# Optimization experiments

Hardware: AMD Instinct MI355X
Metric: run time of the kernel (lower is better)

The kernel has to match this reference:

```python
import jax, jax.numpy as jnp
import numpy as np

BS, T, FIN, FOUT = 8, 1024, 512, 512
ALPHA = 0.1      # leaky relu slope
T_K = 3          # t_ksize (odd); temporal band radius = T_K // 2
S_K = 4          # s_ksize semantic topk
NEG_INF = -9e15


def setup_inputs() -> dict:
    key = jax.random.key(0)
    k1, k2, k3, k4 = jax.random.split(key, 4)
    # xavier-uniform-ish scales (gain 1.414)
    w_lim = 1.414 * np.sqrt(6.0 / (FIN + FOUT))
    a_lim = 1.414 * np.sqrt(6.0 / (2 * FOUT + 1))
    return {
        "x_a": jax.random.normal(k1, (BS, T, FIN), jnp.float32),
        "x_v": jax.random.normal(k2, (BS, T, FIN), jnp.float32),
        "W": jax.random.uniform(k3, (FIN, FOUT), jnp.float32, -w_lim, w_lim),
        "a": jax.random.uniform(k4, (2 * FOUT, 1), jnp.float32, -a_lim, a_lim),
    }


def _temporal_mask(t):
    # tem_adj[i,j] = 1 iff |i-j| <= T_K//2 and i, j on the same side of t-0.5
    idx = jnp.arange(2 * t)
    same_side = (idx[:, None] >= t) == (idx[None, :] >= t)
    band = jnp.abs(idx[:, None] - idx[None, :]) <= (T_K // 2)
    return band & same_side  # (2t, 2t) bool


def _semantic_block_mask(x, k):
    # x: (bs, t, d). Top-k neighbors by negative squared euclidean distance.
    inner = 2.0 * jnp.einsum("btd,bsd->bts", x, x)
    sq = jnp.sum(x * x, axis=-1, keepdims=True)  # (bs, t, 1)
    pd = -(sq - inner + jnp.swapaxes(sq, -1, -2))  # (bs, t, t)
    _, idx = jax.lax.top_k(pd, k)  # (bs, t, k)
    bs, t = x.shape[0], x.shape[1]
    b_ix = jnp.arange(bs)[:, None, None]
    r_ix = jnp.arange(t)[None, :, None]
    return jnp.zeros((bs, t, t), bool).at[b_ix, r_ix, idx].set(True)


def reference(x_a, x_v, W, a):
    bs, t, _ = x_a.shape
    h = jnp.concatenate([x_a, x_v], axis=1)          # (bs, 2t, FIN)
    Wh = h @ W                                        # (bs, 2t, FOUT)

    # additive GAT score: e = leakyrelu(Wh a1 + (Wh a2)^T)
    Wh1 = Wh @ a[:FOUT]                               # (bs, 2t, 1)
    Wh2 = Wh @ a[FOUT:]                               # (bs, 2t, 1)
    e = Wh1 + jnp.swapaxes(Wh2, -1, -2)               # (bs, 2t, 2t)
    e = jnp.where(e > 0, e, ALPHA * e)                # leaky relu

    # adjacency: temporal band + semantic topk within aa / vv blocks
    tem = _temporal_mask(t)                           # (2t, 2t)
    sem_aa = _semantic_block_mask(Wh[:, :t], S_K)     # (bs, t, t)
    sem_vv = _semantic_block_mask(Wh[:, t:], S_K)     # (bs, t, t)
    zb = jnp.zeros((bs, t, t), bool)
    sem = jnp.concatenate([
        jnp.concatenate([sem_aa, zb], axis=-1),
        jnp.concatenate([zb, sem_vv], axis=-1),
    ], axis=1)                                        # (bs, 2t, 2t)
    mask = tem[None] | sem

    attention = jax.nn.softmax(jnp.where(mask, e, NEG_INF), axis=-1)
    h_prime = jax.nn.elu(attention @ Wh)              # (bs, 2t, FOUT)
    return h_prime[:, :t], h_prime[:, t:]
```

## Files before the change

### kernel.cpp

```cpp
#include <hip/hip_runtime.h>
#include <math.h>

#define T_ 1024
#define BS_ 8
#define D_ 512
#define NROWS_ (BS_*2*T_)
#define ALPHA_ 0.1f

typedef _Float16 f16;
typedef _Float16 f16x8 __attribute__((ext_vector_type(8)));
typedef _Float16 f16x4 __attribute__((ext_vector_type(4)));
typedef _Float16 f16x2 __attribute__((ext_vector_type(2)));
typedef float f32x4 __attribute__((ext_vector_type(4)));

#define MFMA16(A,B,C) __builtin_amdgcn_mfma_f32_16x16x32_f16((A),(B),(C),0,0,0)

__device__ __forceinline__ void gl16(const void* g, void* l) {
    __builtin_amdgcn_global_load_lds(
        (const __attribute__((address_space(1))) unsigned int*)g,
        (__attribute__((address_space(3))) unsigned int*)l, 16, 0, 0);
}

#if __has_builtin(__builtin_amdgcn_fdot2)
__device__ __forceinline__ float fdot2p(f16x2 a, f16x2 b, float c) {
    return __builtin_amdgcn_fdot2(a, b, c, false);
}
#else
__device__ __forceinline__ float fdot2p(f16x2 a, f16x2 b, float c) {
    return fmaf((float)a[1], (float)b[1], fmaf((float)a[0], (float)b[0], c));
}
#endif

__device__ __forceinline__ float fdot8(const f16x8 a, const f16x8 b, float s) {
    #pragma unroll
    for (int q = 0; q < 4; ++q) {
        f16x2 aa, bb;
        aa[0] = a[2*q]; aa[1] = a[2*q+1];
        bb[0] = b[2*q]; bb[1] = b[2*q+1];
        s = fdot2p(aa, bb, s);
    }
    return s;
}

__device__ __forceinline__ unsigned sortable(float f) {
    unsigned u = __float_as_uint(f);
    return u ^ ((u & 0x80000000u) ? 0xFFFFFFFFu : 0x80000000u);
}
__device__ __forceinline__ unsigned pack_key(float s, int col) {
    return (sortable(s) & 0xFFFFFC00u) | (unsigned)(1023 - col);
}

#define INSK4(K, X) { \
    bool g3 = (X) > K[3], g2 = (X) > K[2], g1 = (X) > K[1], g0 = (X) > K[0]; \
    K[3] = g2 ? K[2] : (g3 ? (X) : K[3]); \
    K[2] = g1 ? K[1] : (g2 ? (X) : K[2]); \
    K[1] = g0 ? K[0] : (g1 ? (X) : K[1]); \
    K[0] = g0 ? (X) : K[0]; }

#define INSK8(K, X) { \
    bool h7=(X)>K[7],h6=(X)>K[6],h5=(X)>K[5],h4=(X)>K[4]; \
    bool h3=(X)>K[3],h2=(X)>K[2],h1=(X)>K[1],h0=(X)>K[0]; \
    K[7]=h6?K[6]:(h7?(X):K[7]); K[6]=h5?K[5]:(h6?(X):K[6]); \
    K[5]=h4?K[4]:(h5?(X):K[5]); K[4]=h3?K[3]:(h4?(X):K[4]); \
    K[3]=h2?K[2]:(h3?(X):K[3]); K[2]=h1?K[1]:(h2?(X):K[2]); \
    K[1]=h0?K[0]:(h1?(X):K[1]); K[0]=h0?(X):K[0]; }

#define CEU(a,b) { unsigned mx_ = (a) > (b) ? (a) : (b); \
    unsigned mn_ = (a) > (b) ? (b) : (a); (a) = mx_; (b) = mn_; }

#define MERGE8(K, MSK) { \
    unsigned b0=__shfl_xor(K[0],MSK), b1=__shfl_xor(K[1],MSK), \
             b2=__shfl_xor(K[2],MSK), b3=__shfl_xor(K[3],MSK), \
             b4=__shfl_xor(K[4],MSK), b5=__shfl_xor(K[5],MSK), \
             b6=__shfl_xor(K[6],MSK), b7=__shfl_xor(K[7],MSK); \
    K[0]=K[0]>b7?K[0]:b7; K[1]=K[1]>b6?K[1]:b6; \
    K[2]=K[2]>b5?K[2]:b5; K[3]=K[3]>b4?K[3]:b4; \
    K[4]=K[4]>b3?K[4]:b3; K[5]=K[5]>b2?K[5]:b2; \
    K[6]=K[6]>b1?K[6]:b1; K[7]=K[7]>b0?K[7]:b0; \
    CEU(K[0],K[4]); CEU(K[1],K[5]); CEU(K[2],K[6]); CEU(K[3],K[7]); \
    CEU(K[0],K[2]); CEU(K[1],K[3]); CEU(K[4],K[6]); CEU(K[5],K[7]); \
    CEU(K[0],K[1]); CEU(K[2],K[3]); CEU(K[4],K[5]); CEU(K[6],K[7]); }

#define BETTER(x,xi,v,vi) ((x) > (v) || ((x) == (v) && (xi) < (vi)))
#define INS4T(TV,TI,X,ID) { \
    bool g3 = BETTER(X,ID,TV[3],TI[3]), g2 = BETTER(X,ID,TV[2],TI[2]); \
    bool g1 = BETTER(X,ID,TV[1],TI[1]), g0 = BETTER(X,ID,TV[0],TI[0]); \
    TV[3] = g2 ? TV[2] : (g3 ? (X) : TV[3]); TI[3] = g2 ? TI[2] : (g3 ? (ID) : TI[3]); \
    TV[2] = g1 ? TV[1] : (g2 ? (X) : TV[2]); TI[2] = g1 ? TI[1] : (g2 ? (ID) : TI[2]); \
    TV[1] = g0 ? TV[0] : (g1 ? (X) : TV[1]); TI[1] = g0 ? TI[0] : (g1 ? (ID) : TI[1]); \
    TV[0] = g0 ? (X) : TV[0]; TI[0] = g0 ? (ID) : TI[0]; }

__global__ __launch_bounds__(256) void k_splitW(
    const float* __restrict__ W, f16* __restrict__ WTh, f16* __restrict__ WTl)
{
    __shared__ float tile[64][65];
    const int tid = threadIdx.x;
    const int tk = (blockIdx.x >> 3) << 6, tn = (blockIdx.x & 7) << 6;
    const int r0 = tid >> 4, c4 = (tid & 15) << 2;

    #pragma unroll
    for (int rr = 0; rr < 4; ++rr) {
        int k = r0 + (rr << 4);
        float4 v = *(const float4*)(W + (size_t)(tk + k) * D_ + tn + c4);
        tile[k][c4+0] = v.x; tile[k][c4+1] = v.y;
        tile[k][c4+2] = v.z; tile[k][c4+3] = v.w;
    }
    __syncthreads();
    #pragma unroll
    for (int rr = 0; rr < 4; ++rr) {
        int n = r0 + (rr << 4);
        f16x4 h, l;
        #pragma unroll
        for (int i = 0; i < 4; ++i) {
            float x = tile[c4 + i][n];
            f16 hh = (f16)x; h[i] = hh; l[i] = (f16)(x - (float)hh);
        }
        *(f16x4*)(WTh + (size_t)(tn + n) * D_ + tk + c4) = h;
        *(f16x4*)(WTl + (size_t)(tn + n) * D_ + tk + c4) = l;
    }
}

__global__ __launch_bounds__(512, 4) void k_gemm_wh(
    const float* __restrict__ xa, const float* __restrict__ xv,
    const f16* __restrict__ WTh, const f16* __restrict__ WTl,
    const float* __restrict__ a,
    f16* __restrict__ Whh, f16* __restrict__ Whl,
    float* __restrict__ stP)
{
    __shared__ __align__(16) unsigned char smem[69632];

    const int tid  = threadIdx.x;
    const int w    = tid >> 6;
    const int wr   = w >> 2, wc = w & 3;
    const int lane = tid & 63;
    const int l15  = lane & 15;
    const int g    = lane >> 4;
    const int bid  = blockIdx.x;
    const int swz  = ((bid & 7) << 6) + (bid >> 3);
    const int rowbase = (swz >> 1) << 6;
    const int nt   = swz & 1;

    if (tid < 256)
        *(float4*)(smem + 65536 + (tid << 4)) = *(const float4*)(a + (tid << 2));

    const int qp = rowbase >> 10;
    const float* xsrc = ((qp & 1) ? xv : xa)
                      + (size_t)((qp >> 1) * 1024 + (rowbase & 1023)) * D_;
    const int arow = (wr << 5) + l15;

    const char* WThB = (const char*)WTh;
    const char* WTlB = (const char*)WTl;

    const int col0 = tid >> 3;
    const int j80  = (tid & 7) ^ (col0 & 7);

    const int bo0 = (((wc << 5) +  0 + l15) << 7) + ((g ^ (l15 & 7)) << 4);
    const int bo1 = (((wc << 5) + 16 + l15) << 7) + ((g ^ (l15 & 7)) << 4);

    #define STAGE_B(t_) { \
        const int kc_ = (t_) >> 1, cq_ = (t_) & 1; \
        const int bufb_ = ((t_) & 1) << 15; \
        const size_t g0_ = ((size_t)((nt << 8) + (cq_ << 7) + col0) << 10) + ((size_t)kc_ << 7) + (j80 << 4); \
        const size_t g1_ = g0_ + ((size_t)64 << 10); \
        gl16(WThB + g0_, smem + bufb_ + (tid << 4)); \
        gl16(WThB + g1_, smem + bufb_ + ((tid + 512) << 4)); \
        gl16(WTlB + g0_, smem + bufb_ + 16384 + (tid << 4)); \
        gl16(WTlB + g1_, smem + bufb_ + 16384 + ((tid + 512) << 4)); }

    #define LOAD_A(dst_, kc_) { \
        _Pragma("unroll") \
        for (int r_ = 0; r_ < 2; ++r_) { \
            const float* p_ = xsrc + (size_t)(arow + (r_ << 4)) * D_ + ((kc_) << 6) + (g << 3); \
            dst_[(r_ << 2) + 0] = *(const float4*)(p_); \
            dst_[(r_ << 2) + 1] = *(const float4*)(p_ + 4); \
            dst_[(r_ << 2) + 2] = *(const float4*)(p_ + 32); \
            dst_[(r_ << 2) + 3] = *(const float4*)(p_ + 36); } }

    #define CONV_A(src_) { \
        _Pragma("unroll") \
        for (int r_ = 0; r_ < 2; ++r_) \
        _Pragma("unroll") \
        for (int s_ = 0; s_ < 2; ++s_) { \
            float4 v0_ = src_[(r_ << 2) + (s_ << 1)]; \
            float4 v1_ = src_[(r_ << 2) + (s_ << 1) + 1]; \
            float xs_[8] = {v0_.x,v0_.y,v0_.z,v0_.w,v1_.x,v1_.y,v1_.z,v1_.w}; \
            f16x8 h_, l_; \
            _Pragma("unroll") \
            for (int e_ = 0; e_ < 8; ++e_) { \
                f16 hh_ = (f16)xs_[e_]; h_[e_] = hh_; l_[e_] = (f16)(xs_[e_] - (float)hh_); } \
            AH[r_][s_] = h_; AL[r_][s_] = l_; } }

    f32x4 acc[2][2][2];
    #pragma unroll
    for (int cq = 0; cq < 2; ++cq)
        #pragma unroll
        for (int m = 0; m < 2; ++m)
            #pragma unroll
            for (int c = 0; c < 2; ++c) acc[cq][m][c] = (f32x4){0.f,0.f,0.f,0.f};

    float4 aR[8];
    f16x8 AH[2][2], AL[2][2];

    LOAD_A(aR, 0);
    STAGE_B(0);

    #pragma unroll
    for (int t = 0; t < 16; ++t) {
        const int kc = t >> 1, cq = t & 1, bufb = (t & 1) << 15;
        __syncthreads();
        if (t < 15) STAGE_B(t + 1);
        if (cq == 0) { CONV_A(aR); }
        else if (kc < 7) { LOAD_A(aR, kc + 1); }

        #pragma unroll
        for (int s = 0; s < 2; ++s) {
            const int sx = s << 6;
            f16x8 bh0 = *(const f16x8*)(smem + bufb + (bo0 ^ sx));
            f16x8 bh1 = *(const f16x8*)(smem + bufb + (bo1 ^ sx));
            f16x8 bl0 = *(const f16x8*)(smem + bufb + 16384 + (bo0 ^ sx));
            f16x8 bl1 = *(const f16x8*)(smem + bufb + 16384 + (bo1 ^ sx));

            acc[cq][0][0] = MFMA16(AH[0][s], bh0, acc[cq][0][0]);
            acc[cq][0][1] = MFMA16(AH[0][s], bh1, acc[cq][0][1]);
            acc[cq][1][0] = MFMA16(AH[1][s], bh0, acc[cq][1][0]);
            acc[cq][1][1] = MFMA16(AH[1][s], bh1, acc[cq][1][1]);
            acc[cq][0][0] = MFMA16(AL[0][s], bh0, acc[cq][0][0]);
            acc[cq][0][1] = MFMA16(AL[0][s], bh1, acc[cq][0][1]);
            acc[cq][1][0] = MFMA16(AL[1][s], bh0, acc[cq][1][0]);
            acc[cq][1][1] = MFMA16(AL[1][s], bh1, acc[cq][1][1]);
            acc[cq][0][0] = MFMA16(AH[0][s], bl0, acc[cq][0][0]);
            acc[cq][0][1] = MFMA16(AH[0][s], bl1, acc[cq][0][1]);
            acc[cq][1][0] = MFMA16(AH[1][s], bl0, acc[cq][1][0]);
            acc[cq][1][1] = MFMA16(AH[1][s], bl1, acc[cq][1][1]);
        }
    }
    #undef STAGE_B
    #undef LOAD_A
    #undef CONV_A

    __syncthreads();

    float st1[8], st2[8], stq[8];
    #pragma unroll
    for (int s = 0; s < 8; ++s) { st1[s] = 0.f; st2[s] = 0.f; stq[s] = 0.f; }

    #pragma unroll
    for (int cq = 0; cq < 2; ++cq)
        #pragma unroll
        for (int c = 0; c < 2; ++c) {
            const int col = (nt << 8) + (cq << 7) + (wc << 5) + (c << 4) + l15;
            const float a1 = *(const float*)(smem + 65536 + (col << 2));
            const float a2 = *(const float*)(smem + 65536 + 2048 + (col << 2));
            #pragma unroll
            for (int m = 0; m < 2; ++m)
                #pragma unroll
                for (int j = 0; j < 4; ++j) {
                    const float v = acc[cq][m][c][j];
                    const int slot = (m << 2) + j;
                    st1[slot] = fmaf(v, a1, st1[slot]);
                    st2[slot] = fmaf(v, a2, st2[slot]);
                    stq[slot] = fmaf(v, v,  stq[slot]);
                    f16 h = (f16)v; f16 l = (f16)(v - (float)h);
                    const size_t off = (size_t)(rowbase + (wr << 5) + (m << 4) + (g << 2) + j) * D_ + col;
                    Whh[off] = h; Whl[off] = l;
                }
        }

    #pragma unroll
    for (int mask = 1; mask < 16; mask <<= 1)
        #pragma unroll
        for (int s = 0; s < 8; ++s) {
            st1[s] += __shfl_xor(st1[s], mask);
            st2[s] += __shfl_xor(st2[s], mask);
            stq[s] += __shfl_xor(stq[s], mask);
        }
    if (l15 == 0) {
        #pragma unroll
        for (int s = 0; s < 8; ++s) {
            const int rl = (wr << 5) + ((s >> 2) << 4) + (g << 2) + (s & 3);
            float* sp = (float*)smem + ((rl << 2) + wc) * 3;
            sp[0] = st1[s]; sp[1] = st2[s]; sp[2] = stq[s];
        }
    }
    __syncthreads();
    if (tid < 64) {
        float s1 = 0.f, s2 = 0.f, s3 = 0.f;
        #pragma unroll
        for (int wv = 0; wv < 4; ++wv) {
            const float* sp = (const float*)smem + ((tid << 2) + wv) * 3;
            s1 += sp[0]; s2 += sp[1]; s3 += sp[2];
        }
        float* base = stP + (size_t)nt * 3 * NROWS_;
        base[rowbase + tid]              = s1;
        base[NROWS_ + rowbase + tid]     = s2;
        base[2 * NROWS_ + rowbase + tid] = s3;
    }
}

__global__ __launch_bounds__(256) void k_stats(
    const float* __restrict__ stP, float* __restrict__ Wh1,
    float* __restrict__ Wh2, float* __restrict__ sq)
{
    const int i = (blockIdx.x << 8) + threadIdx.x;
    const float* p0 = stP;
    const float* p1 = stP + 3 * NROWS_;
    Wh1[i] = p0[i] + p1[i];
    Wh2[i] = p0[NROWS_ + i] + p1[NROWS_ + i];
    sq[i]  = p0[2 * NROWS_ + i] + p1[2 * NROWS_ + i];
}

__global__ __launch_bounds__(512, 1) void k_gram_topk8(
    const f16* __restrict__ Whh, const float* __restrict__ sq,
    int* __restrict__ topk8)
{
    __shared__ __align__(16) unsigned char smem[81920];

    const int bid = blockIdx.x;
    const int swz = ((bid & 7) << 5) + (bid >> 3);
    const int p   = swz >> 4;
    const int rt  = swz & 15;
    const int rowbase  = (p << 10) + (rt << 6);
    const int colPanel = p << 10;

    const int tid  = threadIdx.x;
    const int w    = tid >> 6;
    const int wr   = w >> 2, wc = w & 3;
    const int lane = tid & 63;
    const int l15  = lane & 15;
    const int g    = lane >> 4;
    const int r8   = lane >> 3;
    const int k7   = lane & 7;
    const int sw2  = ((k7 ^ r8) << 4);
    const int q0x  = ((g ^ (lane & 7)) << 4);

    const int rowA = tid >> 3;
    const int k7A  = tid & 7;
    const int aswz = ((k7A ^ (rowA & 7)) << 4);

    const char* WB = (const char*)Whh;

    const int aoff0 = 32768 + (((wr << 5) +  0 + l15) << 7) + q0x;
    const int aoff1 = 32768 + (((wr << 5) + 16 + l15) << 7) + q0x;
    const int boff0 = (((wc << 6) +  0 + l15) << 7) + q0x;
    const int boff1 = (((wc << 6) + 16 + l15) << 7) + q0x;
    const int boff2 = (((wc << 6) + 32 + l15) << 7) + q0x;
    const int boff3 = (((wc << 6) + 48 + l15) << 7) + q0x;

    f32x4 acc[2][4];
    #pragma unroll
    for (int m = 0; m < 2; ++m)
        #pragma unroll
        for (int c = 0; c < 4; ++c) acc[m][c] = (f32x4){0.f,0.f,0.f,0.f};

    unsigned k4[8][4];
    #pragma unroll
    for (int s = 0; s < 8; ++s)
        #pragma unroll
        for (int q = 0; q < 4; ++q) k4[s][q] = 0u;

    #define STAGE_G(t) { \
        const int ct_ = (t) >> 3, kc_ = (t) & 7; \
        const int bufb_ = ((t) & 1) * 40960; \
        size_t gB_ = ((size_t)(colPanel + (ct_ << 8) + (w << 5) + r8) << 10) + (kc_ << 7) + sw2; \
        int ldsB_ = bufb_ + (w << 12) + (lane << 4); \
        _Pragma("unroll") \
        for (int j_ = 0; j_ < 4; ++j_) { \
            gl16(WB + gB_, smem + ldsB_); \
            gB_ += (size_t)8 << 10; ldsB_ += 1024; \
        } \
        size_t gA_ = ((size_t)(rowbase + rowA) << 10) + (kc_ << 7) + aswz; \
        gl16(WB + gA_, smem + bufb_ + 32768 + (tid << 4)); \
    }

    STAGE_G(0);

    for (int t = 0; t < 32; ++t) {
        __syncthreads();
        if (t < 31) STAGE_G(t + 1);
        const int bufb = (t & 1) * 40960;

        #pragma unroll
        for (int s = 0; s < 2; ++s) {
            const int sx = s << 6;
            f16x8 a0 = *(const f16x8*)(smem + bufb + (aoff0 ^ sx));
            f16x8 a1 = *(const f16x8*)(smem + bufb + (aoff1 ^ sx));
            f16x8 b0 = *(const f16x8*)(smem + bufb + (boff0 ^ sx));
            f16x8 b1 = *(const f16x8*)(smem + bufb + (boff1 ^ sx));
            f16x8 b2 = *(const f16x8*)(smem + bufb + (boff2 ^ sx));
            f16x8 b3 = *(const f16x8*)(smem + bufb + (boff3 ^ sx));
            acc[0][0] = MFMA16(a0, b0, acc[0][0]);
            acc[0][1] = MFMA16(a0, b1, acc[0][1]);
            acc[0][2] = MFMA16(a0, b2, acc[0][2]);
            acc[0][3] = MFMA16(a0, b3, acc[0][3]);
            acc[1][0] = MFMA16(a1, b0, acc[1][0]);
            acc[1][1] = MFMA16(a1, b1, acc[1][1]);
            acc[1][2] = MFMA16(a1, b2, acc[1][2]);
            acc[1][3] = MFMA16(a1, b3, acc[1][3]);
        }

        if ((t & 7) == 7) {
            const int ct = t >> 3;
            #pragma unroll
            for (int c = 0; c < 4; ++c) {
                const int cl = (ct << 8) + (wc << 6) + (c << 4) + l15;
                const float sqc = sq[colPanel + cl];
                #pragma unroll
                for (int m = 0; m < 2; ++m)
                    #pragma unroll
                    for (int j = 0; j < 4; ++j) {
                        float sc = fmaf(2.f, acc[m][c][j], -sqc);
                        unsigned key = pack_key(sc, cl);
                        INSK4(k4[(m << 2) + j], key);
                    }
                acc[0][c] = (f32x4){0.f,0.f,0.f,0.f};
                acc[1][c] = (f32x4){0.f,0.f,0.f,0.f};
            }
        }
    }

    unsigned k8[8][8];
    #pragma unroll
    for (int s = 0; s < 8; ++s) {
        #pragma unroll
        for (int q = 0; q < 4; ++q) { k8[s][q] = k4[s][q]; k8[s][4 + q] = 0u; }
    }
    #pragma unroll
    for (int msk = 1; msk < 16; msk <<= 1) {
        #pragma unroll
        for (int s = 0; s < 8; ++s) { MERGE8(k8[s], msk); }
    }

    if (l15 == 0) {
        #pragma unroll
        for (int s = 0; s < 8; ++s) {
            const int row_local = ((s >> 2) << 4) + (g << 2) + (s & 3);
            const int off = ((((wr << 5) + row_local) << 2) + wc) << 5;
            *(uint4*)(smem + off)      = make_uint4(k8[s][0], k8[s][1], k8[s][2], k8[s][3]);
            *(uint4*)(smem + off + 16) = make_uint4(k8[s][4], k8[s][5], k8[s][6], k8[s][7]);
        }
    }
    __syncthreads();
    if (tid < 64) {
        const unsigned* bp = (const unsigned*)smem + (tid << 5);
        unsigned kk[8];
        #pragma unroll
        for (int s = 0; s < 8; ++s) kk[s] = bp[s];
        #pragma unroll
        for (int wv = 1; wv < 4; ++wv)
            #pragma unroll
            for (int s = 0; s < 8; ++s) { unsigned x = bp[(wv << 3) + s]; INSK8(kk, x); }
        #pragma unroll
        for (int s = 0; s < 8; ++s)
            topk8[(((size_t)(rowbase + tid)) << 3) + s] = 1023 - (int)(kk[s] & 1023u);
    }
    #undef STAGE_G
}

__global__ __launch_bounds__(256) void k_rescore_agg(
    const f16* __restrict__ Whh, const f16* __restrict__ Whl,
    const float* __restrict__ Wh1, const float* __restrict__ Wh2,
    const float* __restrict__ sq, const int* __restrict__ topk8,
    float* __restrict__ out)
{
    const int bid = blockIdx.x;
    const int swz = ((bid & 7) << 9) + (bid >> 3);
    const int tid  = threadIdx.x;
    const int lane = tid & 63;
    const int r    = (swz << 2) + (tid >> 6);
    const int p    = r >> 10;
    const int i    = r & 1023;
    const int rb   = p << 10;

    const size_t ro = (size_t)r * D_ + (lane << 3);
    f16x8 ah = *(const f16x8*)(Whh + ro);
    f16x8 al = *(const f16x8*)(Whl + ro);

    int cid[8];
    {
        int4 t0 = *(const int4*)(topk8 + ((size_t)r << 3));
        int4 t1 = *(const int4*)(topk8 + ((size_t)r << 3) + 4);
        cid[0]=t0.x; cid[1]=t0.y; cid[2]=t0.z; cid[3]=t0.w;
        cid[4]=t1.x; cid[5]=t1.y; cid[6]=t1.z; cid[7]=t1.w;
    }

    float dp[8];
    #pragma unroll
    for (int c = 0; c < 8; ++c) {
        const size_t co = (size_t)(rb + cid[c]) * D_ + (lane << 3);
        f16x8 bh = *(const f16x8*)(Whh + co);
        f16x8 bl = *(const f16x8*)(Whl + co);
        float s = 0.f;
        s = fdot8(ah, bh, s);
        s = fdot8(ah, bl, s);
        s = fdot8(al, bh, s);
        dp[c] = s;
    }
    #pragma unroll
    for (int off = 32; off > 0; off >>= 1)
        #pragma unroll
        for (int c = 0; c < 8; ++c) dp[c] += __shfl_xor(dp[c], off);

    float tv[4] = {-3.4e38f,-3.4e38f,-3.4e38f,-3.4e38f};
    int   ti[4] = {0x7FFFFFFF,0x7FFFFFFF,0x7FFFFFFF,0x7FFFFFFF};
    #pragma unroll
    for (int c = 0; c < 8; ++c) {
        float sc = fmaf(2.f, dp[c], -sq[rb + cid[c]]);
        INS4T(tv, ti, sc, cid[c]);
    }

    const int  tM = i - 1, tC = i, tP = i + 1;
    const bool vM = (i > 0), vP = (i < T_ - 1);
    const int s0 = ti[0], s1 = ti[1], s2 = ti[2], s3 = ti[3];

    bool u0 = !((vM && s0 == tM) || (s0 == tC) || (vP && s0 == tP));
    bool u1 = !((vM && s1 == tM) || (s1 == tC) || (vP && s1 == tP));
    bool u2 = !((vM && s2 == tM) || (s2 == tC) || (vP && s2 == tP));
    bool u3 = !((vM && s3 == tM) || (s3 == tC) || (vP && s3 == tP));

    int  ci[7] = { vM ? tM : 0, tC, vP ? tP : 0, s0, s1, s2, s3 };
    bool cv[7] = { vM, true, vP, u0, u1, u2, u3 };

    const float e1 = Wh1[r];
    float ev[7];
    float m = -3.4e38f;
    #pragma unroll
    for (int q = 0; q < 7; ++q) {
        float e = e1 + Wh2[rb + ci[q]];
        e = (e > 0.f) ? e : ALPHA_ * e;
        e = cv[q] ? e : -3.4e38f;
        ev[q] = e;
        m = fmaxf(m, e);
    }
    float wsum = 0.f;
    #pragma unroll
    for (int q = 0; q < 7; ++q) {
        float wq = cv[q] ? expf(ev[q] - m) : 0.f;
        ev[q] = wq;
        wsum += wq;
    }
    #pragma unroll
    for (int q = 0; q < 7; ++q) ev[q] /= wsum;

    float A[8] = {0.f,0.f,0.f,0.f,0.f,0.f,0.f,0.f};
    #pragma unroll
    for (int q = 0; q < 7; ++q) {
        if (ev[q] > 0.f) {
            const float wq = ev[q];
            const size_t qo = (size_t)(rb + ci[q]) * D_ + (lane << 3);
            f16x8 vh = *(const f16x8*)(Whh + qo);
            f16x8 vl = *(const f16x8*)(Whl + qo);
            #pragma unroll
            for (int e = 0; e < 8; ++e) A[e] = fmaf(wq, (float)vh[e], A[e]);
            #pragma unroll
            for (int e = 0; e < 8; ++e) A[e] = fmaf(wq, (float)vl[e], A[e]);
        }
    }
    #pragma unroll
    for (int e = 0; e < 8; ++e)
        A[e] = (A[e] > 0.f) ? A[e] : expm1f(A[e]);

    const int blk = p & 1, b = p >> 1;
    float* dst = out + (size_t)blk * ((size_t)BS_ * T_ * D_)
               + ((size_t)((b << 10) + i)) * D_ + (lane << 3);
    *(float4*)(dst)     = make_float4(A[0], A[1], A[2], A[3]);
    *(float4*)(dst + 4) = make_float4(A[4], A[5], A[6], A[7]);
}

extern "C" void kernel_launch(void* const* d_in, const int* in_sizes, int n_in,
                              void* d_out, int out_size, void* d_ws, size_t ws_size,
                              hipStream_t stream)
{
    const float* xa = (const float*)d_in[0];
    const float* xv = (const float*)d_in[1];
    const float* W  = (const float*)d_in[2];
    const float* a  = (const float*)d_in[3];
    float* out = (float*)d_out;

    f16* Whh    = (f16*)d_ws;
    f16* Whl    = Whh + (size_t)NROWS_ * D_;
    f16* WTh    = Whl + (size_t)NROWS_ * D_;
    f16* WTl    = WTh + (size_t)D_ * D_;
    float* Wh1  = (float*)(WTl + (size_t)D_ * D_);
    float* Wh2  = Wh1 + NROWS_;
    float* sq   = Wh2 + NROWS_;
    int* topk8  = (int*)(sq + NROWS_);
    float* stP  = (float*)(topk8 + ((size_t)NROWS_ << 3));

    k_splitW     <<<dim3(64),   dim3(256), 0, stream>>>(W, WTh, WTl);
    k_gemm_wh    <<<dim3(512),  dim3(512), 0, stream>>>(xa, xv, WTh, WTl, a, Whh, Whl, stP);
    k_stats      <<<dim3(64),   dim3(256), 0, stream>>>(stP, Wh1, Wh2, sq);
    k_gram_topk8 <<<dim3(256),  dim3(512), 0, stream>>>(Whh, sq, topk8);
    k_rescore_agg<<<dim3(4096), dim3(256), 0, stream>>>(Whh, Whl, Wh1, Wh2, sq, topk8, out);
}
```

Measured before the change: 131.6 us.

## Widen GEMM tile to full 512 columns and drop separate stats kernel

Each GEMM block now computes a 64-row by full 512-column tile instead of half the columns, so per-row statistics (Wh·a1, Wh·a2, squared norm) are reduced entirely inside the block and the separate k_stats kernel and partial-stat buffer go away. The A operand is now converted to hi/lo fp16 once and staged through LDS, shared across both column halves, rather than held in registers per wave. The aim is to halve redundant A loads and conversions and remove one launch. In exchange the grid halves to 256 blocks, LDS use and registers per block grow, and occupancy bounds drop to 2 blocks per CU.

```diff
diff --git a/kernel.cpp b/kernel.cpp
--- a/kernel.cpp
+++ b/kernel.cpp
@@ -120,14 +120,14 @@
     }
 }
 
-__global__ __launch_bounds__(512, 4) void k_gemm_wh(
+__global__ __launch_bounds__(512, 2) void k_gemm_wh(
     const float* __restrict__ xa, const float* __restrict__ xv,
     const f16* __restrict__ WTh, const f16* __restrict__ WTl,
     const float* __restrict__ a,
     f16* __restrict__ Whh, f16* __restrict__ Whl,
-    float* __restrict__ stP)
+    float* __restrict__ Wh1, float* __restrict__ Wh2, float* __restrict__ sq)
 {
-    __shared__ __align__(16) unsigned char smem[69632];
+    __shared__ __align__(16) unsigned char smem[86016];
 
     const int tid  = threadIdx.x;
     const int w    = tid >> 6;
@@ -136,135 +136,146 @@
     const int l15  = lane & 15;
     const int g    = lane >> 4;
     const int bid  = blockIdx.x;
-    const int swz  = ((bid & 7) << 6) + (bid >> 3);
-    const int rowbase = (swz >> 1) << 6;
-    const int nt   = swz & 1;
+    const int swz  = ((bid & 7) << 5) + (bid >> 3);
+    const int rowbase = swz << 6;
 
     if (tid < 256)
-        *(float4*)(smem + 65536 + (tid << 4)) = *(const float4*)(a + (tid << 2));
+        *(float4*)(smem + 81920 + (tid << 4)) = *(const float4*)(a + (tid << 2));
 
     const int qp = rowbase >> 10;
     const float* xsrc = ((qp & 1) ? xv : xa)
                       + (size_t)((qp >> 1) * 1024 + (rowbase & 1023)) * D_;
-    const int arow = (wr << 5) + l15;
 
     const char* WThB = (const char*)WTh;
     const char* WTlB = (const char*)WTl;
 
-    const int col0 = tid >> 3;
-    const int j80  = (tid & 7) ^ (col0 & 7);
-
-    const int bo0 = (((wc << 5) +  0 + l15) << 7) + ((g ^ (l15 & 7)) << 4);
-    const int bo1 = (((wc << 5) + 16 + l15) << 7) + ((g ^ (l15 & 7)) << 4);
-
-    #define STAGE_B(t_) { \
-        const int kc_ = (t_) >> 1, cq_ = (t_) & 1; \
-        const int bufb_ = ((t_) & 1) << 15; \
-        const size_t g0_ = ((size_t)((nt << 8) + (cq_ << 7) + col0) << 10) + ((size_t)kc_ << 7) + (j80 << 4); \
-        const size_t g1_ = g0_ + ((size_t)64 << 10); \
-        gl16(WThB + g0_, smem + bufb_ + (tid << 4)); \
-        gl16(WThB + g1_, smem + bufb_ + ((tid + 512) << 4)); \
-        gl16(WTlB + g0_, smem + bufb_ + 16384 + (tid << 4)); \
-        gl16(WTlB + g1_, smem + bufb_ + 16384 + ((tid + 512) << 4)); }
-
-    #define LOAD_A(dst_, kc_) { \
+    const int rB1 = tid >> 2,         cB1 = tid & 3;
+    const int jB1 = cB1 ^ ((rB1 >> 1) & 3);
+    const int rB2 = (tid + 512) >> 2, cB2 = tid & 3;
+    const int jB2 = cB2 ^ ((rB2 >> 1) & 3);
+
+    const int rowA = tid >> 3, c8 = tid & 7;
+    const int aW = (rowA << 6) + ((((c8 >> 1) ^ ((rowA >> 1) & 3)) << 4)) + ((c8 & 1) << 3);
+
+    const int swzx = (g ^ ((l15 >> 1) & 3)) << 4;
+    const int ao0 = (((wr << 5) + l15) << 6) + swzx;
+    const int ao1 = ao0 + 1024;
+    const int bo0 = (((wc << 6) +  0 + l15) << 6) + swzx;
+    const int bo1 = (((wc << 6) + 16 + l15) << 6) + swzx;
+    const int bo2 = (((wc << 6) + 32 + l15) << 6) + swzx;
+    const int bo3 = (((wc << 6) + 48 + l15) << 6) + swzx;
+
+    #define STAGE_B(cq_, kc_, bufb_) { \
+        size_t g1_ = ((size_t)(((cq_) << 8) + rB1) << 10) + ((size_t)(kc_) << 6) + (jB1 << 4); \
+        size_t g2_ = ((size_t)(((cq_) << 8) + rB2) << 10) + ((size_t)(kc_) << 6) + (jB2 << 4); \
+        gl16(WThB + g1_, smem + (bufb_) + (tid << 4)); \
+        gl16(WThB + g2_, smem + (bufb_) + ((tid + 512) << 4)); \
+        gl16(WTlB + g1_, smem + (bufb_) + 16384 + (tid << 4)); \
+        gl16(WTlB + g2_, smem + (bufb_) + 16384 + ((tid + 512) << 4)); }
+
+    #define STAGE_A(kc_) { \
+        float4 v_ = *(const float4*)(xsrc + (size_t)rowA * D_ + ((kc_) << 5) + (c8 << 2)); \
+        float xs_[4] = {v_.x, v_.y, v_.z, v_.w}; \
+        f16x4 h_, l_; \
         _Pragma("unroll") \
-        for (int r_ = 0; r_ < 2; ++r_) { \
-            const float* p_ = xsrc + (size_t)(arow + (r_ << 4)) * D_ + ((kc_) << 6) + (g << 3); \
-            dst_[(r_ << 2) + 0] = *(const float4*)(p_); \
-            dst_[(r_ << 2) + 1] = *(const float4*)(p_ + 4); \
-            dst_[(r_ << 2) + 2] = *(const float4*)(p_ + 32); \
-            dst_[(r_ << 2) + 3] = *(const float4*)(p_ + 36); } }
-
-    #define CONV_A(src_) { \
+        for (int e_ = 0; e_ < 4; ++e_) { \
+            f16 hh_ = (f16)xs_[e_]; h_[e_] = hh_; l_[e_] = (f16)(xs_[e_] - (float)hh_); } \
+        const int ab_ = 65536 + (((kc_) & 1) << 13); \
+        *(f16x4*)(smem + ab_ + aW)        = h_; \
+        *(f16x4*)(smem + ab_ + 4096 + aW) = l_; }
+
+    #define COMPUTE(ACC, BUFB, AB) { \
+        f16x8 ah0 = *(const f16x8*)(smem + (AB) + ao0); \
+        f16x8 ah1 = *(const f16x8*)(smem + (AB) + ao1); \
+        f16x8 al0 = *(const f16x8*)(smem + (AB) + 4096 + ao0); \
+        f16x8 al1 = *(const f16x8*)(smem + (AB) + 4096 + ao1); \
+        f16x8 bh0 = *(const f16x8*)(smem + (BUFB) + bo0); \
+        f16x8 bh1 = *(const f16x8*)(smem + (BUFB) + bo1); \
+        f16x8 bh2 = *(const f16x8*)(smem + (BUFB) + bo2); \
+        f16x8 bh3 = *(const f16x8*)(smem + (BUFB) + bo3); \
+        f16x8 bl0 = *(const f16x8*)(smem + (BUFB) + 16384 + bo0); \
+        f16x8 bl1 = *(const f16x8*)(smem + (BUFB) + 16384 + bo1); \
+        f16x8 bl2 = *(const f16x8*)(smem + (BUFB) + 16384 + bo2); \
+        f16x8 bl3 = *(const f16x8*)(smem + (BUFB) + 16384 + bo3); \
+        ACC[0][0] = MFMA16(ah0, bh0, ACC[0][0]); \
+        ACC[0][1] = MFMA16(ah0, bh1, ACC[0][1]); \
+        ACC[0][2] = MFMA16(ah0, bh2, ACC[0][2]); \
+        ACC[0][3] = MFMA16(ah0, bh3, ACC[0][3]); \
+        ACC[1][0] = MFMA16(ah1, bh0, ACC[1][0]); \
+        ACC[1][1] = MFMA16(ah1, bh1, ACC[1][1]); \
+        ACC[1][2] = MFMA16(ah1, bh2, ACC[1][2]); \
+        ACC[1][3] = MFMA16(ah1, bh3, ACC[1][3]); \
+        ACC[0][0] = MFMA16(al0, bh0, ACC[0][0]); \
+        ACC[0][1] = MFMA16(al0, bh1, ACC[0][1]); \
+        ACC[0][2] = MFMA16(al0, bh2, ACC[0][2]); \
+        ACC[0][3] = MFMA16(al0, bh3, ACC[0][3]); \
+        ACC[1][0] = MFMA16(al1, bh0, ACC[1][0]); \
+        ACC[1][1] = MFMA16(al1, bh1, ACC[1][1]); \
+        ACC[1][2] = MFMA16(al1, bh2, ACC[1][2]); \
+        ACC[1][3] = MFMA16(al1, bh3, ACC[1][3]); \
+        ACC[0][0] = MFMA16(ah0, bl0, ACC[0][0]); \
+        ACC[0][1] = MFMA16(ah0, bl1, ACC[0][1]); \
+        ACC[0][2] = MFMA16(ah0, bl2, ACC[0][2]); \
+        ACC[0][3] = MFMA16(ah0, bl3, ACC[0][3]); \
+        ACC[1][0] = MFMA16(ah1, bl0, ACC[1][0]); \
+        ACC[1][1] = MFMA16(ah1, bl1, ACC[1][1]); \
+        ACC[1][2] = MFMA16(ah1, bl2, ACC[1][2]); \
+        ACC[1][3] = MFMA16(ah1, bl3, ACC[1][3]); }
+
+    f32x4 acc0[2][4], acc1[2][4];
+    #pragma unroll
+    for (int m = 0; m < 2; ++m)
+        #pragma unroll
+        for (int c = 0; c < 4; ++c) {
+            acc0[m][c] = (f32x4){0.f,0.f,0.f,0.f};
+            acc1[m][c] = (f32x4){0.f,0.f,0.f,0.f};
+        }
+
+    STAGE_A(0);
+    STAGE_B(0, 0, 0);
+
+    for (int kk = 0; kk < 16; ++kk) {
+        const int ab = 65536 + ((kk & 1) << 13);
+        __syncthreads();
+        STAGE_B(1, kk, 32768);
+        COMPUTE(acc0, 0, ab);
+        __syncthreads();
+        if (kk < 15) { STAGE_B(0, kk + 1, 0); STAGE_A(kk + 1); }
+        COMPUTE(acc1, 32768, ab);
+    }
+    #undef STAGE_B
+    #undef STAGE_A
+    #undef COMPUTE
+
+    __syncthreads();
+
+    float st1[8], st2[8], stq[8];
+    #pragma unroll
+    for (int s = 0; s < 8; ++s) { st1[s] = 0.f; st2[s] = 0.f; stq[s] = 0.f; }
+
+    #define EPI(ACC, CQ) { \
         _Pragma("unroll") \
-        for (int r_ = 0; r_ < 2; ++r_) \
-        _Pragma("unroll") \
-        for (int s_ = 0; s_ < 2; ++s_) { \
-            float4 v0_ = src_[(r_ << 2) + (s_ << 1)]; \
-            float4 v1_ = src_[(r_ << 2) + (s_ << 1) + 1]; \
-            float xs_[8] = {v0_.x,v0_.y,v0_.z,v0_.w,v1_.x,v1_.y,v1_.z,v1_.w}; \
-            f16x8 h_, l_; \
+        for (int c = 0; c < 4; ++c) { \
+            const int col = ((CQ) << 8) + (wc << 6) + (c << 4) + l15; \
+            const float a1 = *(const float*)(smem + 81920 + (col << 2)); \
+            const float a2 = *(const float*)(smem + 81920 + 2048 + (col << 2)); \
             _Pragma("unroll") \
-            for (int e_ = 0; e_ < 8; ++e_) { \
-                f16 hh_ = (f16)xs_[e_]; h_[e_] = hh_; l_[e_] = (f16)(xs_[e_] - (float)hh_); } \
-            AH[r_][s_] = h_; AL[r_][s_] = l_; } }
-
-    f32x4 acc[2][2][2];
-    #pragma unroll
-    for (int cq = 0; cq < 2; ++cq)
-        #pragma unroll
-        for (int m = 0; m < 2; ++m)
-            #pragma unroll
-            for (int c = 0; c < 2; ++c) acc[cq][m][c] = (f32x4){0.f,0.f,0.f,0.f};
-
-    float4 aR[8];
-    f16x8 AH[2][2], AL[2][2];
-
-    LOAD_A(aR, 0);
-    STAGE_B(0);
-
-    #pragma unroll
-    for (int t = 0; t < 16; ++t) {
-        const int kc = t >> 1, cq = t & 1, bufb = (t & 1) << 15;
-        __syncthreads();
-        if (t < 15) STAGE_B(t + 1);
-        if (cq == 0) { CONV_A(aR); }
-        else if (kc < 7) { LOAD_A(aR, kc + 1); }
-
-        #pragma unroll
-        for (int s = 0; s < 2; ++s) {
-            const int sx = s << 6;
-            f16x8 bh0 = *(const f16x8*)(smem + bufb + (bo0 ^ sx));
-            f16x8 bh1 = *(const f16x8*)(smem + bufb + (bo1 ^ sx));
-            f16x8 bl0 = *(const f16x8*)(smem + bufb + 16384 + (bo0 ^ sx));
-            f16x8 bl1 = *(const f16x8*)(smem + bufb + 16384 + (bo1 ^ sx));
-
-            acc[cq][0][0] = MFMA16(AH[0][s], bh0, acc[cq][0][0]);
-            acc[cq][0][1] = MFMA16(AH[0][s], bh1, acc[cq][0][1]);
-            acc[cq][1][0] = MFMA16(AH[1][s], bh0, acc[cq][1][0]);
-            acc[cq][1][1] = MFMA16(AH[1][s], bh1, acc[cq][1][1]);
-            acc[cq][0][0] = MFMA16(AL[0][s], bh0, acc[cq][0][0]);
-            acc[cq][0][1] = MFMA16(AL[0][s], bh1, acc[cq][0][1]);
-            acc[cq][1][0] = MFMA16(AL[1][s], bh0, acc[cq][1][0]);
-            acc[cq][1][1] = MFMA16(AL[1][s], bh1, acc[cq][1][1]);
-            acc[cq][0][0] = MFMA16(AH[0][s], bl0, acc[cq][0][0]);
-            acc[cq][0][1] = MFMA16(AH[0][s], bl1, acc[cq][0][1]);
-            acc[cq][1][0] = MFMA16(AH[1][s], bl0, acc[cq][1][0]);
-            acc[cq][1][1] = MFMA16(AH[1][s], bl1, acc[cq][1][1]);
-        }
-    }
-    #undef STAGE_B
-    #undef LOAD_A
-    #undef CONV_A
-
-    __syncthreads();
-
-    float st1[8], st2[8], stq[8];
-    #pragma unroll
-    for (int s = 0; s < 8; ++s) { st1[s] = 0.f; st2[s] = 0.f; stq[s] = 0.f; }
-
-    #pragma unroll
-    for (int cq = 0; cq < 2; ++cq)
-        #pragma unroll
-        for (int c = 0; c < 2; ++c) {
-            const int col = (nt << 8) + (cq << 7) + (wc << 5) + (c << 4) + l15;
-            const float a1 = *(const float*)(smem + 65536 + (col << 2));
-            const float a2 = *(const float*)(smem + 65536 + 2048 + (col << 2));
-            #pragma unroll
-            for (int m = 0; m < 2; ++m)
-                #pragma unroll
-                for (int j = 0; j < 4; ++j) {
-                    const float v = acc[cq][m][c][j];
-                    const int slot = (m << 2) + j;
-                    st1[slot] = fmaf(v, a1, st1[slot]);
-                    st2[slot] = fmaf(v, a2, st2[slot]);
-                    stq[slot] = fmaf(v, v,  stq[slot]);
-                    f16 h = (f16)v; f16 l = (f16)(v - (float)h);
-                    const size_t off = (size_t)(rowbase + (wr << 5) + (m << 4) + (g << 2) + j) * D_ + col;
-                    Whh[off] = h; Whl[off] = l;
-                }
-        }
+            for (int m = 0; m < 2; ++m) \
+            _Pragma("unroll") \
+            for (int j = 0; j < 4; ++j) { \
+                const float v = ACC[m][c][j]; \
+                const int slot = (m << 2) + j; \
+                st1[slot] = fmaf(v, a1, st1[slot]); \
+                st2[slot] = fmaf(v, a2, st2[slot]); \
+                stq[slot] = fmaf(v, v,  stq[slot]); \
+                f16 h = (f16)v; f16 l = (f16)(v - (float)h); \
+                const size_t off = (size_t)(rowbase + (wr << 5) + (m << 4) + (g << 2) + j) * D_ + col; \
+                Whh[off] = h; Whl[off] = l; \
+            } } }
+
+    EPI(acc0, 0);
+    EPI(acc1, 1);
+    #undef EPI
 
     #pragma unroll
     for (int mask = 1; mask < 16; mask <<= 1)
@@ -290,23 +301,8 @@
             const float* sp = (const float*)smem + ((tid << 2) + wv) * 3;
             s1 += sp[0]; s2 += sp[1]; s3 += sp[2];
         }
-        float* base = stP + (size_t)nt * 3 * NROWS_;
-        base[rowbase + tid]              = s1;
-        base[NROWS_ + rowbase + tid]     = s2;
-        base[2 * NROWS_ + rowbase + tid] = s3;
-    }
-}
-
-__global__ __launch_bounds__(256) void k_stats(
-    const float* __restrict__ stP, float* __restrict__ Wh1,
-    float* __restrict__ Wh2, float* __restrict__ sq)
-{
-    const int i = (blockIdx.x << 8) + threadIdx.x;
-    const float* p0 = stP;
-    const float* p1 = stP + 3 * NROWS_;
-    Wh1[i] = p0[i] + p1[i];
-    Wh2[i] = p0[NROWS_ + i] + p1[NROWS_ + i];
-    sq[i]  = p0[2 * NROWS_ + i] + p1[2 * NROWS_ + i];
+        Wh1[rowbase + tid] = s1; Wh2[rowbase + tid] = s2; sq[rowbase + tid] = s3;
+    }
 }
 
 __global__ __launch_bounds__(512, 1) void k_gram_topk8(
@@ -584,11 +580,9 @@
     float* Wh2  = Wh1 + NROWS_;
     float* sq   = Wh2 + NROWS_;
     int* topk8  = (int*)(sq + NROWS_);
-    float* stP  = (float*)(topk8 + ((size_t)NROWS_ << 3));
 
     k_splitW     <<<dim3(64),   dim3(256), 0, stream>>>(W, WTh, WTl);
-    k_gemm_wh    <<<dim3(512),  dim3(512), 0, stream>>>(xa, xv, WTh, WTl, a, Whh, Whl, stP);
-    k_stats      <<<dim3(64),   dim3(256), 0, stream>>>(stP, Wh1, Wh2, sq);
+    k_gemm_wh    <<<dim3(256),  dim3(512), 0, stream>>>(xa, xv, WTh, WTl, a, Whh, Whl, Wh1, Wh2, sq);
     k_gram_topk8 <<<dim3(256),  dim3(512), 0, stream>>>(Whh, sq, topk8);
     k_rescore_agg<<<dim3(4096), dim3(256), 0, stream>>>(Whh, Whl, Wh1, Wh2, sq, topk8, out);
 }
```

Result: faster. 124.1 us (-5.7%).
